# Performance work log

Hardware: AMD Instinct MI355X
Metric: run time of the kernel (lower is better)

Reference implementation:

```python
import jax, jax.numpy as jnp
import numpy as np

H = 128          # hidden_size
GX = GY = 512    # grid_size
SW = 2           # spatial_width
NX = GX + 3 * SW # memory extent x (as in SpatialExternalMemory ctor)
NY = GY + 3 * SW
B = 512          # batch (num trajectories)
T = 64           # seq len (recurrent steps)


def setup_inputs() -> dict:
    key = jax.random.key(0)
    ks = jax.random.split(key, 9)
    stdv = 1.0 / np.sqrt(H)
    feat = jax.random.normal(ks[0], (B, T, 2), jnp.float32)
    # integer grid coords stored as floats in cols 2:4 (cast to long in forward)
    coords = jax.random.randint(ks[1], (B, T, 2), 0, GX).astype(jnp.float32)
    feature_tensor = jnp.concatenate([feat, coords], axis=-1)  # [B, T, 4]
    seq_lengths = jax.random.randint(ks[2], (B,), 1, T + 1)
    uni = lambda k, shp: jax.random.uniform(k, shp, jnp.float32, -stdv, stdv)
    return {
        "feature_tensor": feature_tensor,
        "W_ih": uni(ks[3], (4 * H, 2)),
        "b_ih": uni(ks[4], (4 * H,)),
        "W_hh": uni(ks[5], (4 * H, H)),
        "b_hh": uni(ks[6], (4 * H,)),
        "W_out": uni(ks[7], (H, 2 * H)),   # Attention.linear_out: [H, 2H]
        "b_out": uni(ks[8], (H,)),
        "seq_lengths": seq_lengths,
    }


def reference(feature_tensor, W_ih, b_ih, W_hh, b_hh, W_out, b_out, seq_lengths):
    step_idx = jnp.maximum(seq_lengths.astype(jnp.int32), 1) - 1  # [B]
    offsets = jnp.arange(-SW, SW + 1)                              # [K], K=2*SW+1
    K = 2 * SW + 1
    memory0 = jnp.zeros((NX, NY, H), jnp.float32)
    hidden0 = jnp.zeros((B, H), jnp.float32)
    last0 = jnp.zeros((B, H), jnp.float32)

    def step(carry, inp):
        hidden, memory, last = carry
        xt, t = inp                                 # xt: [B,4]
        feat = xt[:, :2]
        grid = xt[:, 2:4].astype(jnp.int32) + SW    # [B,2]
        gi = feat @ W_ih.T + b_ih                   # [B,4H]
        gh = hidden @ W_hh.T + b_hh                 # [B,4H]
        i_r, i_i, i_n, i_s = jnp.split(gi, 4, axis=1)
        h_r, h_i, h_n, h_s = jnp.split(gh, 4, axis=1)
        resetgate = jax.nn.sigmoid(i_r + h_r)
        updategate = jax.nn.sigmoid(i_i + h_i)
        spatialgate = jax.nn.sigmoid(i_s + h_s)
        newgate = jnp.tanh(i_n + resetgate * h_n)
        # --- find_nearby_grids: 5x5 neighborhood gather ---
        gx = jnp.clip(grid[:, 0], 0, NX - 1)
        gy = jnp.clip(grid[:, 1], 0, NY - 1)
        xi = jnp.clip(gx[:, None] + offsets[None, :], 0, NX - 1)   # [B,K]
        yi = jnp.clip(gy[:, None] + offsets[None, :], 0, NY - 1)   # [B,K]
        xg = jnp.broadcast_to(xi[:, :, None], (B, K, K)).reshape(B, K * K)
        yg = jnp.broadcast_to(yi[:, None, :], (B, K, K)).reshape(B, K * K)
        context = memory[xg, yg]                    # [B, K*K, H]
        # --- Attention(newgate.detach(), context) ---
        q = jax.lax.stop_gradient(newgate)
        scores = jnp.einsum('bh,bkh->bk', q, context)
        scores = jnp.where(scores == 0.0, -jnp.inf, scores)
        attn = jax.nn.softmax(scores, axis=1)
        attn = jnp.where(jnp.isnan(attn), 0.0, attn)
        mix = jnp.einsum('bk,bkh->bh', attn, context)
        atten_cs = jnp.tanh(jnp.concatenate([mix, q], axis=-1) @ W_out.T + b_out)
        curr = newgate + spatialgate * atten_cs
        out = curr + updategate * (hidden - curr)
        # --- in-cell memory write (detached, training-mode path) ---
        sd = jax.lax.stop_gradient(spatialgate)
        od = jax.lax.stop_gradient(out)
        upd = sd * memory[gx, gy] + (1.0 - sd) * od
        memory = memory.at[gx, gy].set(upd)
        last = jnp.where((step_idx == t)[:, None], out, last)
        return (out, memory, last), None

    xs = (jnp.swapaxes(feature_tensor, 0, 1), jnp.arange(T))
    (_, _, last), _ = jax.lax.scan(step, (hidden0, memory0, last0), xs)
    return last
```

## Files before the change

kernel.cpp:

```cpp
#include <hip/hip_runtime.h>
#include <hip/hip_fp16.h>
#include <math.h>

#define Hc   128
#define Bc   512
#define Tc   64
#define NXc  518
#define NCELL (518*518)
#define NEV  (Bc*Tc)
#define SWc  2


__global__ void k_build(const float* __restrict__ feat, int* __restrict__ head,
                        int* __restrict__ nxt, int* __restrict__ cellxy) {
    int gid = blockIdx.x * 256 + threadIdx.x;
    if (gid >= NEV) return;
    int b = gid >> 6, t = gid & 63;
    int base = (b * Tc + t) * 4;
    int gx = (int)feat[base + 2] + SWc;
    int gy = (int)feat[base + 3] + SWc;
    gx = min(max(gx, 0), NXc - 1);
    gy = min(max(gy, 0), NXc - 1);
    int cell = gx * NXc + gy;
    int e = t * Bc + b;
    cellxy[e] = (gx << 16) | gy;
    int old = atomicExch(&head[cell], e);
    nxt[e] = old;
}

__global__ void k_resolve(const int* __restrict__ head, const int* __restrict__ nxt,
                          const int* __restrict__ cellxy, int* __restrict__ dep) {
    int gid = blockIdx.x * 256 + threadIdx.x;
    if (gid >= NEV * 25) return;
    int r = gid / 25, k = gid - r * 25;
    int t = r & 63, b = r >> 6;
    int e0 = t * Bc + b;
    int xy = cellxy[e0];
    int gx = xy >> 16, gy = xy & 0xffff;
    int cx = gx + (k / 5) - SWc, cy = gy + (k % 5) - SWc;
    cx = min(max(cx, 0), NXc - 1);
    cy = min(max(cy, 0), NXc - 1);
    int cell = cx * NXc + cy;
    int best = -1;
    for (int e = head[cell]; e >= 0; e = nxt[e])
        if ((e >> 9) < t && e > best) best = e;
    dep[r * 25 + k] = best;
}


#define LOG2E 1.4426950408889634f
__device__ __forceinline__ float fexp(float x)  { return __builtin_amdgcn_exp2f(x * LOG2E); }
__device__ __forceinline__ float fsig(float x)  { return __builtin_amdgcn_rcpf(1.f + fexp(-x)); }
__device__ __forceinline__ float ftanh(float x) { return 1.f - 2.f * __builtin_amdgcn_rcpf(1.f + fexp(2.f * x)); }

template <int CTRL>
__device__ __forceinline__ float dppadd(float x) {
    int t = __builtin_amdgcn_update_dpp(0, __float_as_int(x), CTRL, 0xF, 0xF, true);
    return x + __int_as_float(t);
}
template <int CTRL>
__device__ __forceinline__ float dppmax(float x) {
    int t = __builtin_amdgcn_update_dpp(0, __float_as_int(x), CTRL, 0xF, 0xF, true);
    return fmaxf(x, __int_as_float(t));
}
__device__ __forceinline__ float swz16(float x) {
    return __int_as_float(__builtin_amdgcn_ds_swizzle(__float_as_int(x), 0x401F));
}
__device__ __forceinline__ float redsum64(float d) {
    d = dppadd<0xB1>(d); d = dppadd<0x4E>(d);
    d = dppadd<0x141>(d); d = dppadd<0x140>(d);
    d += swz16(d);
    d += __shfl_xor(d, 32, 64);
    return d;
}

__device__ __forceinline__ void barlds() {
    asm volatile("" ::: "memory");
    __builtin_amdgcn_s_waitcnt(0xC07F);
    __builtin_amdgcn_s_barrier();
    asm volatile("" ::: "memory");
}

__device__ __forceinline__ unsigned flagload(const unsigned* p) {
    return __hip_atomic_load(p, __ATOMIC_RELAXED, __HIP_MEMORY_SCOPE_AGENT);
}


constexpr int LDS_FLOATS = 16512 + 256 + 1024 + 256 + 256 + 64 + 2048 + 512 + 16 + 128 + 256 + 128;
constexpr int LDS_BYTES  = LDS_FLOATS * 4;

__global__ void
__attribute__((amdgpu_flat_work_group_size(1024, 1024)))
__attribute__((amdgpu_waves_per_eu(4, 4)))
step_main(const float* __restrict__ feat, const float* __restrict__ Wih,
          const float* __restrict__ bih,  const float* __restrict__ Whh,
          const float* __restrict__ bhh,  const float* __restrict__ Wout,
          const float* __restrict__ bout, const int*   __restrict__ seq,
          const int*   __restrict__ dep,  float* __restrict__ vbuf,
          unsigned*    __restrict__ flags, float* __restrict__ dout) {
    extern __shared__ float lds[];
    __half2* WoutH = (__half2*)lds;
    float* hid   = lds + 16512;
    float* g     = hid   + 256;
    float* gin   = g     + 1024;
    float* ctr   = gin   + 256;
    float* scor  = ctr   + 256;
    float* pmix  = scor  + 64;
    float* catL  = pmix  + 2048;
    float* fxy   = catL  + 512;
    float* boutL = fxy   + 16;
    float* updL  = boutL + 128;
    int*   depv  = (int*)(updL + 256);

    const int tid  = threadIdx.x;
    const int blk  = blockIdx.x;
    const int lane = tid & 63;
    const int w    = tid >> 6;
    const int wj   = w >> 3;
    const int ww   = w & 7;

    const int rp = tid >> 2;
    const int q  = tid & 3;
    const int r0 = 2 * rp, r1 = 2 * rp + 1;
    float4 wr0[8], wr1[8];
    {
        const float4* w0 = (const float4*)(Whh + (size_t)r0 * Hc);
        const float4* w1 = (const float4*)(Whh + (size_t)r1 * Hc);
        #pragma unroll
        for (int i = 0; i < 8; ++i) { wr0[i] = w0[q + 4 * i]; wr1[i] = w1[q + 4 * i]; }
    }
    #pragma unroll
    for (int i = 0; i < 8; ++i) {
        asm volatile("" : "+v"(wr0[i].x), "+v"(wr0[i].y), "+v"(wr0[i].z), "+v"(wr0[i].w));
        asm volatile("" : "+v"(wr1[i].x), "+v"(wr1[i].y), "+v"(wr1[i].z), "+v"(wr1[i].w));
    }
    const int jw = q & 1;
    const int rw = r0 + (q >> 1);
    const float bihr = bih[rw], bhhr = bhh[rw];
    const float wihA = Wih[rw * 2 + 0], wihB = Wih[rw * 2 + 1];
    const int chunk = rw >> 7;

    for (int i = tid; i < 128 * 128; i += 1024) {
        int r = i >> 7, c2 = i & 127;
        WoutH[r * 129 + c2] = __floats2half2_rn(Wout[r * 256 + 2 * c2],
                                                Wout[r * 256 + 2 * c2 + 1]);
    }
    if (tid < 128) boutL[tid] = bout[tid];
    if (tid < 256) hid[tid] = 0.f;
    if (tid < 8) { int j = tid >> 2, c = tid & 3;
                   fxy[tid] = feat[((size_t)(blk * 2 + j) * Tc + 0) * 4 + c]; }
    if (tid < 50) {
        int j = (tid >= 25), k = tid - j * 25;
        depv[tid] = dep[(((size_t)(blk * 2 + j)) * Tc + 0) * 25 + k];
    }
    const int s0 = max(seq[blk * 2 + 0], 1) - 1;
    const int s1 = max(seq[blk * 2 + 1], 1) - 1;
    __syncthreads();

    const float NEG_INF = -__builtin_inff();

    for (int t = 0; t < Tc; ++t) {
        const float* fx = fxy + (t & 1) * 8;
        int* depvCur = depv + (t & 1) * 64;
        int* depvNxt = depv + ((t + 1) & 1) * 64;

        if (t > 0 && (w == 0 || w == 2)) {
            int j = w >> 1;
            float2 u = *(const float2*)&updL[j * 128 + 2 * lane];
            unsigned long long raw; __builtin_memcpy(&raw, &u, 8);
            __hip_atomic_store((unsigned long long*)(vbuf +
                ((size_t)((t - 1) * Bc + blk * 2 + j)) * Hc + 2 * lane),
                raw, __ATOMIC_RELAXED, __HIP_MEMORY_SCOPE_AGENT);
        }
        const int mye = (lane < 25) ? depvCur[wj * 25 + lane] : -1;
        unsigned fpre = 0u;
        if (mye >= 0)
            fpre = flagload(&flags[mye]);
        unsigned long long rdymask = __ballot((mye >= 0) && (fpre != 0u));
        int evk[4]; bool rdy[4]; float2 valk[4];
        #pragma unroll
        for (int kk = 0; kk < 4; ++kk) {
            int k = ww + 8 * kk;
            evk[kk] = (k < 25) ? depvCur[wj * 25 + k] : -1;
            rdy[kk] = (evk[kk] >= 0) && ((rdymask >> k) & 1ull);
            valk[kk] = make_float2(0.f, 0.f);
        }
        asm volatile("" ::: "memory");
        #pragma unroll
        for (int kk = 0; kk < 4; ++kk)
            if (rdy[kk])
                valk[kk] = *(const float2*)(vbuf + (size_t)evk[kk] * Hc + 2 * lane);

        float a00 = 0.f, a01 = 0.f, a10 = 0.f, a11 = 0.f;
        {
            const float4* h0 = (const float4*)hid;
            const float4* h1 = (const float4*)(hid + 128);
            #pragma unroll
            for (int i = 0; i < 8; ++i) {
                float4 hv0 = h0[q + 4 * i], hv1 = h1[q + 4 * i];
                float4 w0 = wr0[i], w1 = wr1[i];
                a00 = fmaf(w0.x, hv0.x, fmaf(w0.y, hv0.y, fmaf(w0.z, hv0.z, fmaf(w0.w, hv0.w, a00))));
                a01 = fmaf(w1.x, hv0.x, fmaf(w1.y, hv0.y, fmaf(w1.z, hv0.z, fmaf(w1.w, hv0.w, a01))));
                a10 = fmaf(w0.x, hv1.x, fmaf(w0.y, hv1.y, fmaf(w0.z, hv1.z, fmaf(w0.w, hv1.w, a10))));
                a11 = fmaf(w1.x, hv1.x, fmaf(w1.y, hv1.y, fmaf(w1.z, hv1.z, fmaf(w1.w, hv1.w, a11))));
            }
        }
        a00 = dppadd<0x4E>(dppadd<0xB1>(a00));
        a01 = dppadd<0x4E>(dppadd<0xB1>(a01));
        a10 = dppadd<0x4E>(dppadd<0xB1>(a10));
        a11 = dppadd<0x4E>(dppadd<0xB1>(a11));
        {
            float mine = (q & 1) ? ((q >> 1) ? a11 : a10) : ((q >> 1) ? a01 : a00);
            float gi  = fmaf(wihA, fx[jw * 4 + 0], wihB * fx[jw * 4 + 1]);
            g[jw * 512 + rw] = mine + bhhr + ((chunk == 2) ? 0.f : (gi + bihr));
            if (chunk == 2) gin[jw * 128 + (rw & 127)] = gi + bihr;
        }
        if (tid >= 512 && tid < 562 && t + 1 < Tc) {
            int idx = tid - 512;
            int j = (idx >= 25), k = idx - j * 25;
            depvNxt[idx] = dep[(((size_t)(blk * 2 + j)) * Tc + (t + 1)) * 25 + k];
        }
        if (tid >= 960 && tid < 968 && t + 1 < Tc) {
            int idx = tid - 960, j = idx >> 2, c = idx & 3;
            fxy[((t + 1) & 1) * 8 + idx] =
                feat[((size_t)(blk * 2 + j) * Tc + (t + 1)) * 4 + c];
        }
        if (t > 0 && (w == 0 || w == 2)) {
            asm volatile("s_waitcnt vmcnt(0)" ::: "memory");
            if (lane == 0)
                __hip_atomic_store(&flags[(t - 1) * Bc + blk * 2 + (w >> 1)], 1u,
                                   __ATOMIC_RELAXED, __HIP_MEMORY_SCOPE_AGENT);
        }
        {
            bool pend = (mye >= 0) && (fpre == 0u);
            while (__any(pend)) {
                if (pend && flagload(&flags[mye]) != 0u)
                    pend = false;
                if (__any(pend)) __builtin_amdgcn_s_sleep(1);
            }
            asm volatile("" ::: "memory");
            #pragma unroll
            for (int kk = 0; kk < 4; ++kk)
                if (evk[kk] >= 0 && !rdy[kk])
                    valk[kk] = *(const float2*)(vbuf + (size_t)evk[kk] * Hc + 2 * lane);
        }
        barlds();

        float q0, q1;
        {
            float2 gr2 = *(const float2*)&g[wj * 512 + 2 * lane];
            float2 gn2 = *(const float2*)&g[wj * 512 + 256 + 2 * lane];
            float2 gi2 = *(const float2*)&gin[wj * 128 + 2 * lane];
            q0 = ftanh(gi2.x + fsig(gr2.x) * gn2.x);
            q1 = ftanh(gi2.y + fsig(gr2.y) * gn2.y);
        }
        if (ww == 0) *(float2*)&catL[wj * 256 + 128 + 2 * lane] = make_float2(q0, q1);
        if (ww == 4)
            *(float2*)&ctr[wj * 128 + 2 * lane] =
                (evk[1] >= 0) ? valk[1] : make_float2(0.f, 0.f);
        #pragma unroll
        for (int kk = 0; kk < 4; ++kk) {
            int k = ww + 8 * kk;
            if (k < 25) {
                float sc;
                if (evk[kk] >= 0) {
                    float d = fmaf(valk[kk].x, q0, valk[kk].y * q1);
                    d = redsum64(d);
                    sc = (d == 0.f) ? NEG_INF : d;
                } else sc = NEG_INF;
                if (lane == 0) scor[wj * 32 + k] = sc;
            }
        }
        barlds();

        {
            int k2 = lane & 31;
            float v = (k2 < 25) ? scor[wj * 32 + k2] : NEG_INF;
            float m = v;
            m = dppmax<0xB1>(m); m = dppmax<0x4E>(m);
            m = dppmax<0x141>(m); m = dppmax<0x140>(m);
            m = fmaxf(m, swz16(m));
            float a = 0.f;
            if (m != NEG_INF) {
                float p = (v == NEG_INF) ? 0.f : fexp(v - m);
                float s = p;
                s = dppadd<0xB1>(s); s = dppadd<0x4E>(s);
                s = dppadd<0x141>(s); s = dppadd<0x140>(s);
                s += swz16(s);
                a = p / s;
            }
            float pm0 = 0.f, pm1 = 0.f;
            #pragma unroll
            for (int kk = 0; kk < 4; ++kk) {
                int k = ww + 8 * kk;
                if (k < 25 && evk[kk] >= 0) {
                    float ak = __int_as_float(
                        __builtin_amdgcn_readlane(__float_as_int(a), k));
                    pm0 = fmaf(ak, valk[kk].x, pm0);
                    pm1 = fmaf(ak, valk[kk].y, pm1);
                }
            }
            *(float2*)&pmix[(wj * 8 + ww) * 128 + 2 * lane] = make_float2(pm0, pm1);
        }
        barlds();

        if (tid < 256) {
            int j = tid >> 7, h = tid & 127;
            float mix = 0.f;
            #pragma unroll
            for (int p = 0; p < 8; ++p) mix += pmix[(j * 8 + p) * 128 + h];
            catL[j * 256 + h] = mix;
        }
        barlds();

        {
            int oo = tid & 127, rep = tid >> 7;
            const __half2* wrow = WoutH + oo * 129 + rep * 16;
            const float4* c04 = (const float4*)(catL + rep * 32);
            const float4* c14 = (const float4*)(catL + 256 + rep * 32);
            float acc0 = 0.f, acc1 = 0.f;
            #pragma unroll
            for (int i = 0; i < 8; ++i) {
                __half2 wa = wrow[2 * i], wb = wrow[2 * i + 1];
                float wx = __low2float(wa), wy = __high2float(wa);
                float wz = __low2float(wb), wwv = __high2float(wb);
                float4 c0 = c04[i], c1 = c14[i];
                acc0 = fmaf(wx, c0.x, fmaf(wy, c0.y, fmaf(wz, c0.z, fmaf(wwv, c0.w, acc0))));
                acc1 = fmaf(wx, c1.x, fmaf(wy, c1.y, fmaf(wz, c1.z, fmaf(wwv, c1.w, acc1))));
            }
            pmix[rep * 128 + oo]       = acc0;
            pmix[(8 + rep) * 128 + oo] = acc1;
        }
        barlds();

        if (tid < 256) {
            int j = tid >> 7, h = tid & 127;
            float tot = boutL[h];
            #pragma unroll
            for (int p = 0; p < 8; ++p) tot += pmix[(j * 8 + p) * 128 + h];
            float at = ftanh(tot);
            float gr = g[j * 512 + h],       gu = g[j * 512 + 128 + h];
            float gn = g[j * 512 + 256 + h], gs = g[j * 512 + 384 + h];
            float rr = fsig(gr), uu = fsig(gu), ss = fsig(gs);
            float nn = ftanh(gin[j * 128 + h] + rr * gn);
            float hv = hid[j * 128 + h];
            float curr = fmaf(ss, at, nn);
            float outv = curr + uu * (hv - curr);
            hid[j * 128 + h] = outv;
            if (t < Tc - 1)
                updL[tid] = fmaf(ss, ctr[j * 128 + h], (1.f - ss) * outv);
            int sj = (j == 0) ? s0 : s1;
            if (sj == t) dout[(size_t)(blk * 2 + j) * Hc + h] = outv;
        }
        barlds();
    }
}


extern "C" void kernel_launch(void* const* d_in, const int* in_sizes, int n_in,
                              void* d_out, int out_size, void* d_ws, size_t ws_size,
                              hipStream_t stream) {
    const float* feat = (const float*)d_in[0];
    const float* Wih  = (const float*)d_in[1];
    const float* bih  = (const float*)d_in[2];
    const float* Whh  = (const float*)d_in[3];
    const float* bhh  = (const float*)d_in[4];
    const float* Wout = (const float*)d_in[5];
    const float* bout = (const float*)d_in[6];
    const int*   seq  = (const int*)d_in[7];

    char* ws = (char*)d_ws;
    size_t off = 0;
    auto carve = [&](size_t bytes) { char* p = ws + off; off += (bytes + 511) & ~(size_t)511; return p; };
    float*    vbuf   = (float*)   carve((size_t)NEV * Hc * 4);
    int*      head   = (int*)     carve((size_t)NCELL * 4);
    int*      nxt    = (int*)     carve((size_t)NEV * 4);
    int*      cellxy = (int*)     carve((size_t)NEV * 4);
    int*      dep    = (int*)     carve((size_t)NEV * 25 * 4);
    unsigned* flags  = (unsigned*)carve((size_t)NEV * 4);

    hipMemsetAsync(head, 0xFF, (size_t)NCELL * 4, stream);
    hipMemsetAsync(flags, 0, (size_t)NEV * 4, stream);

    k_build<<<(NEV + 255) / 256, 256, 0, stream>>>(feat, head, nxt, cellxy);
    k_resolve<<<(NEV * 25 + 255) / 256, 256, 0, stream>>>(head, nxt, cellxy, dep);

    hipFuncSetAttribute((const void*)step_main,
                        hipFuncAttributeMaxDynamicSharedMemorySize, LDS_BYTES);
    step_main<<<256, 1024, LDS_BYTES, stream>>>(feat, Wih, bih, Whh, bhh, Wout, bout,
                                                seq, dep, vbuf, flags, (float*)d_out);
}
```

Measured before the change: 473.0 us.

## Keep Wout in registers, regroup Whh matvec, atomically accumulate attention mix

The fp16 copy of W_out moves from LDS into per-thread registers, and the W_hh matvec is regrouped so each thread holds four rows over eight-lane groups with a three-step DPP reduction. The attention mix partials are now summed with LDS atomicAdd into catL, which removes one reduction pass and one barrier per step. The speculative early loading of ready neighbour values before the matvec is dropped, so all vbuf loads happen after the dependency wait. The change lowers LDS traffic and footprint and trims a barrier, but raises register pressure and adds LDS atomic contention.

```diff
diff --git a/kernel.cpp b/kernel.cpp
--- a/kernel.cpp
+++ b/kernel.cpp
@@ -73,6 +73,10 @@
     d += __shfl_xor(d, 32, 64);
     return d;
 }
+__device__ __forceinline__ float redsum8(float d) {
+    d = dppadd<0xB1>(d); d = dppadd<0x4E>(d); d = dppadd<0x141>(d);
+    return d;
+}
 
 __device__ __forceinline__ void barlds() {
     asm volatile("" ::: "memory");
@@ -86,7 +90,7 @@
 }
 
 
-constexpr int LDS_FLOATS = 16512 + 256 + 1024 + 256 + 256 + 64 + 2048 + 512 + 16 + 128 + 256 + 128;
+constexpr int LDS_FLOATS = 256 + 1024 + 256 + 256 + 64 + 2048 + 512 + 16 + 256 + 128;
 constexpr int LDS_BYTES  = LDS_FLOATS * 4;
 
 __global__ void
@@ -99,8 +103,7 @@
           const int*   __restrict__ dep,  float* __restrict__ vbuf,
           unsigned*    __restrict__ flags, float* __restrict__ dout) {
     extern __shared__ float lds[];
-    __half2* WoutH = (__half2*)lds;
-    float* hid   = lds + 16512;
+    float* hid   = lds;
     float* g     = hid   + 256;
     float* gin   = g     + 1024;
     float* ctr   = gin   + 256;
@@ -108,8 +111,7 @@
     float* pmix  = scor  + 64;
     float* catL  = pmix  + 2048;
     float* fxy   = catL  + 512;
-    float* boutL = fxy   + 16;
-    float* updL  = boutL + 128;
+    float* updL  = fxy   + 16;
     int*   depv  = (int*)(updL + 256);
 
     const int tid  = threadIdx.x;
@@ -119,33 +121,44 @@
     const int wj   = w >> 3;
     const int ww   = w & 7;
 
-    const int rp = tid >> 2;
-    const int q  = tid & 3;
-    const int r0 = 2 * rp, r1 = 2 * rp + 1;
-    float4 wr0[8], wr1[8];
+    const int grp = tid >> 3;
+    const int s   = tid & 7;
+    float4 wrr[4][4];
     {
-        const float4* w0 = (const float4*)(Whh + (size_t)r0 * Hc);
-        const float4* w1 = (const float4*)(Whh + (size_t)r1 * Hc);
-        #pragma unroll
-        for (int i = 0; i < 8; ++i) { wr0[i] = w0[q + 4 * i]; wr1[i] = w1[q + 4 * i]; }
+        const float4* wb = (const float4*)Whh;
+        #pragma unroll
+        for (int r = 0; r < 4; ++r)
+            #pragma unroll
+            for (int i = 0; i < 4; ++i)
+                wrr[r][i] = wb[(size_t)(4 * grp + r) * 32 + s + 8 * i];
     }
     #pragma unroll
-    for (int i = 0; i < 8; ++i) {
-        asm volatile("" : "+v"(wr0[i].x), "+v"(wr0[i].y), "+v"(wr0[i].z), "+v"(wr0[i].w));
-        asm volatile("" : "+v"(wr1[i].x), "+v"(wr1[i].y), "+v"(wr1[i].z), "+v"(wr1[i].w));
+    for (int r = 0; r < 4; ++r)
+        #pragma unroll
+        for (int i = 0; i < 4; ++i)
+            asm volatile("" : "+v"(wrr[r][i].x), "+v"(wrr[r][i].y),
+                              "+v"(wrr[r][i].z), "+v"(wrr[r][i].w));
+
+    const int jwl = s >> 2;
+    const int rwl = 4 * grp + (s & 3);
+    const float bihr = bih[rwl], bhhr = bhh[rwl];
+    const float wihA = Wih[rwl * 2 + 0], wihB = Wih[rwl * 2 + 1];
+    const int chunk = rwl >> 7;
+
+    const int oo7 = tid & 127, rep7 = tid >> 7;
+    unsigned wo[16];
+    {
+        const float* wrow = Wout + (size_t)oo7 * 256 + rep7 * 32;
+        #pragma unroll
+        for (int m = 0; m < 16; ++m) {
+            __half2 hh = __floats2half2_rn(wrow[2 * m], wrow[2 * m + 1]);
+            unsigned u; __builtin_memcpy(&u, &hh, 4);
+            wo[m] = u;
+            asm volatile("" : "+v"(wo[m]));
+        }
     }
-    const int jw = q & 1;
-    const int rw = r0 + (q >> 1);
-    const float bihr = bih[rw], bhhr = bhh[rw];
-    const float wihA = Wih[rw * 2 + 0], wihB = Wih[rw * 2 + 1];
-    const int chunk = rw >> 7;
-
-    for (int i = tid; i < 128 * 128; i += 1024) {
-        int r = i >> 7, c2 = i & 127;
-        WoutH[r * 129 + c2] = __floats2half2_rn(Wout[r * 256 + 2 * c2],
-                                                Wout[r * 256 + 2 * c2 + 1]);
-    }
-    if (tid < 128) boutL[tid] = bout[tid];
+    const float boutr = bout[oo7];
+
     if (tid < 256) hid[tid] = 0.f;
     if (tid < 8) { int j = tid >> 2, c = tid & 3;
                    fxy[tid] = feat[((size_t)(blk * 2 + j) * Tc + 0) * 4 + c]; }
@@ -173,47 +186,41 @@
                 raw, __ATOMIC_RELAXED, __HIP_MEMORY_SCOPE_AGENT);
         }
         const int mye = (lane < 25) ? depvCur[wj * 25 + lane] : -1;
-        unsigned fpre = 0u;
+        unsigned fpre = 1u;
         if (mye >= 0)
             fpre = flagload(&flags[mye]);
-        unsigned long long rdymask = __ballot((mye >= 0) && (fpre != 0u));
-        int evk[4]; bool rdy[4]; float2 valk[4];
-        #pragma unroll
-        for (int kk = 0; kk < 4; ++kk) {
-            int k = ww + 8 * kk;
-            evk[kk] = (k < 25) ? depvCur[wj * 25 + k] : -1;
-            rdy[kk] = (evk[kk] >= 0) && ((rdymask >> k) & 1ull);
-            valk[kk] = make_float2(0.f, 0.f);
-        }
-        asm volatile("" ::: "memory");
-        #pragma unroll
-        for (int kk = 0; kk < 4; ++kk)
-            if (rdy[kk])
-                valk[kk] = *(const float2*)(vbuf + (size_t)evk[kk] * Hc + 2 * lane);
-
-        float a00 = 0.f, a01 = 0.f, a10 = 0.f, a11 = 0.f;
+
+        float acc[2][4];
+        #pragma unroll
+        for (int j = 0; j < 2; ++j) {
+            const float4* hp = (const float4*)(hid + j * 128);
+            float4 h0 = hp[s], h1 = hp[s + 8], h2 = hp[s + 16], h3 = hp[s + 24];
+            #pragma unroll
+            for (int r = 0; r < 4; ++r) {
+                float4 w0 = wrr[r][0], w1 = wrr[r][1], w2 = wrr[r][2], w3 = wrr[r][3];
+                float a = 0.f;
+                a = fmaf(w0.x, h0.x, fmaf(w0.y, h0.y, fmaf(w0.z, h0.z, fmaf(w0.w, h0.w, a))));
+                a = fmaf(w1.x, h1.x, fmaf(w1.y, h1.y, fmaf(w1.z, h1.z, fmaf(w1.w, h1.w, a))));
+                a = fmaf(w2.x, h2.x, fmaf(w2.y, h2.y, fmaf(w2.z, h2.z, fmaf(w2.w, h2.w, a))));
+                a = fmaf(w3.x, h3.x, fmaf(w3.y, h3.y, fmaf(w3.z, h3.z, fmaf(w3.w, h3.w, a))));
+                acc[j][r] = a;
+            }
+        }
+        #pragma unroll
+        for (int j = 0; j < 2; ++j)
+            #pragma unroll
+            for (int r = 0; r < 4; ++r)
+                acc[j][r] = redsum8(acc[j][r]);
         {
-            const float4* h0 = (const float4*)hid;
-            const float4* h1 = (const float4*)(hid + 128);
-            #pragma unroll
-            for (int i = 0; i < 8; ++i) {
-                float4 hv0 = h0[q + 4 * i], hv1 = h1[q + 4 * i];
-                float4 w0 = wr0[i], w1 = wr1[i];
-                a00 = fmaf(w0.x, hv0.x, fmaf(w0.y, hv0.y, fmaf(w0.z, hv0.z, fmaf(w0.w, hv0.w, a00))));
-                a01 = fmaf(w1.x, hv0.x, fmaf(w1.y, hv0.y, fmaf(w1.z, hv0.z, fmaf(w1.w, hv0.w, a01))));
-                a10 = fmaf(w0.x, hv1.x, fmaf(w0.y, hv1.y, fmaf(w0.z, hv1.z, fmaf(w0.w, hv1.w, a10))));
-                a11 = fmaf(w1.x, hv1.x, fmaf(w1.y, hv1.y, fmaf(w1.z, hv1.z, fmaf(w1.w, hv1.w, a11))));
-            }
-        }
-        a00 = dppadd<0x4E>(dppadd<0xB1>(a00));
-        a01 = dppadd<0x4E>(dppadd<0xB1>(a01));
-        a10 = dppadd<0x4E>(dppadd<0xB1>(a10));
-        a11 = dppadd<0x4E>(dppadd<0xB1>(a11));
-        {
-            float mine = (q & 1) ? ((q >> 1) ? a11 : a10) : ((q >> 1) ? a01 : a00);
-            float gi  = fmaf(wihA, fx[jw * 4 + 0], wihB * fx[jw * 4 + 1]);
-            g[jw * 512 + rw] = mine + bhhr + ((chunk == 2) ? 0.f : (gi + bihr));
-            if (chunk == 2) gin[jw * 128 + (rw & 127)] = gi + bihr;
+            int sb = s & 3;
+            float m0 = (sb == 0) ? acc[0][0] : (sb == 1) ? acc[0][1]
+                     : (sb == 2) ? acc[0][2] : acc[0][3];
+            float m1 = (sb == 0) ? acc[1][0] : (sb == 1) ? acc[1][1]
+                     : (sb == 2) ? acc[1][2] : acc[1][3];
+            float mine = jwl ? m1 : m0;
+            float gi = fmaf(wihA, fx[jwl * 4 + 0], wihB * fx[jwl * 4 + 1]);
+            g[jwl * 512 + rwl] = mine + bhhr + ((chunk == 2) ? 0.f : (gi + bihr));
+            if (chunk == 2) gin[jwl * 128 + (rwl & 127)] = gi + bihr;
         }
         if (tid >= 512 && tid < 562 && t + 1 < Tc) {
             int idx = tid - 512;
@@ -238,11 +245,17 @@
                     pend = false;
                 if (__any(pend)) __builtin_amdgcn_s_sleep(1);
             }
-            asm volatile("" ::: "memory");
-            #pragma unroll
-            for (int kk = 0; kk < 4; ++kk)
-                if (evk[kk] >= 0 && !rdy[kk])
-                    valk[kk] = *(const float2*)(vbuf + (size_t)evk[kk] * Hc + 2 * lane);
+        }
+        asm volatile("" ::: "memory");
+        float2 valk[4];
+        int    evk[4];
+        #pragma unroll
+        for (int kk = 0; kk < 4; ++kk) {
+            int k = ww + 8 * kk;
+            evk[kk] = (k < 25) ? depvCur[wj * 25 + k] : -1;
+            valk[kk] = make_float2(0.f, 0.f);
+            if (evk[kk] >= 0)
+                valk[kk] = *(const float2*)(vbuf + (size_t)evk[kk] * Hc + 2 * lane);
         }
         barlds();
 
@@ -255,6 +268,7 @@
             q1 = ftanh(gi2.y + fsig(gr2.y) * gn2.y);
         }
         if (ww == 0) *(float2*)&catL[wj * 256 + 128 + 2 * lane] = make_float2(q0, q1);
+        if (ww == 1) *(float2*)&catL[wj * 256 + 2 * lane] = make_float2(0.f, 0.f);
         if (ww == 4)
             *(float2*)&ctr[wj * 128 + 2 * lane] =
                 (evk[1] >= 0) ? valk[1] : make_float2(0.f, 0.f);
@@ -283,59 +297,53 @@
             float a = 0.f;
             if (m != NEG_INF) {
                 float p = (v == NEG_INF) ? 0.f : fexp(v - m);
-                float s = p;
-                s = dppadd<0xB1>(s); s = dppadd<0x4E>(s);
-                s = dppadd<0x141>(s); s = dppadd<0x140>(s);
-                s += swz16(s);
-                a = p / s;
-            }
-            float pm0 = 0.f, pm1 = 0.f;
-            #pragma unroll
-            for (int kk = 0; kk < 4; ++kk) {
-                int k = ww + 8 * kk;
-                if (k < 25 && evk[kk] >= 0) {
-                    float ak = __int_as_float(
-                        __builtin_amdgcn_readlane(__float_as_int(a), k));
-                    pm0 = fmaf(ak, valk[kk].x, pm0);
-                    pm1 = fmaf(ak, valk[kk].y, pm1);
+                float ssum = p;
+                ssum = dppadd<0xB1>(ssum); ssum = dppadd<0x4E>(ssum);
+                ssum = dppadd<0x141>(ssum); ssum = dppadd<0x140>(ssum);
+                ssum += swz16(ssum);
+                a = p / ssum;
+            }
+            if ((evk[0] >= 0) | (evk[1] >= 0) | (evk[2] >= 0) | (evk[3] >= 0)) {
+                float pm0 = 0.f, pm1 = 0.f;
+                #pragma unroll
+                for (int kk = 0; kk < 4; ++kk) {
+                    int k = ww + 8 * kk;
+                    if (k < 25 && evk[kk] >= 0) {
+                        float ak = __int_as_float(
+                            __builtin_amdgcn_readlane(__float_as_int(a), k));
+                        pm0 = fmaf(ak, valk[kk].x, pm0);
+                        pm1 = fmaf(ak, valk[kk].y, pm1);
+                    }
                 }
-            }
-            *(float2*)&pmix[(wj * 8 + ww) * 128 + 2 * lane] = make_float2(pm0, pm1);
+                atomicAdd(&catL[wj * 256 + 2 * lane],     pm0);
+                atomicAdd(&catL[wj * 256 + 2 * lane + 1], pm1);
+            }
         }
         barlds();
 
-        if (tid < 256) {
-            int j = tid >> 7, h = tid & 127;
-            float mix = 0.f;
-            #pragma unroll
-            for (int p = 0; p < 8; ++p) mix += pmix[(j * 8 + p) * 128 + h];
-            catL[j * 256 + h] = mix;
-        }
-        barlds();
-
         {
-            int oo = tid & 127, rep = tid >> 7;
-            const __half2* wrow = WoutH + oo * 129 + rep * 16;
-            const float4* c04 = (const float4*)(catL + rep * 32);
-            const float4* c14 = (const float4*)(catL + 256 + rep * 32);
+            const float4* c04 = (const float4*)(catL + rep7 * 32);
+            const float4* c14 = (const float4*)(catL + 256 + rep7 * 32);
             float acc0 = 0.f, acc1 = 0.f;
             #pragma unroll
             for (int i = 0; i < 8; ++i) {
-                __half2 wa = wrow[2 * i], wb = wrow[2 * i + 1];
+                unsigned ua = wo[2 * i], ub = wo[2 * i + 1];
+                __half2 wa, wb2;
+                __builtin_memcpy(&wa, &ua, 4); __builtin_memcpy(&wb2, &ub, 4);
                 float wx = __low2float(wa), wy = __high2float(wa);
-                float wz = __low2float(wb), wwv = __high2float(wb);
+                float wz = __low2float(wb2), wv = __high2float(wb2);
                 float4 c0 = c04[i], c1 = c14[i];
-                acc0 = fmaf(wx, c0.x, fmaf(wy, c0.y, fmaf(wz, c0.z, fmaf(wwv, c0.w, acc0))));
-                acc1 = fmaf(wx, c1.x, fmaf(wy, c1.y, fmaf(wz, c1.z, fmaf(wwv, c1.w, acc1))));
-            }
-            pmix[rep * 128 + oo]       = acc0;
-            pmix[(8 + rep) * 128 + oo] = acc1;
+                acc0 = fmaf(wx, c0.x, fmaf(wy, c0.y, fmaf(wz, c0.z, fmaf(wv, c0.w, acc0))));
+                acc1 = fmaf(wx, c1.x, fmaf(wy, c1.y, fmaf(wz, c1.z, fmaf(wv, c1.w, acc1))));
+            }
+            pmix[rep7 * 128 + oo7]       = acc0;
+            pmix[(8 + rep7) * 128 + oo7] = acc1;
         }
         barlds();
 
         if (tid < 256) {
             int j = tid >> 7, h = tid & 127;
-            float tot = boutL[h];
+            float tot = boutr;
             #pragma unroll
             for (int p = 0; p < 8; ++p) tot += pmix[(j * 8 + p) * 128 + h];
             float at = ftanh(tot);
```

New measurement: 486.0 us. 2.8% more time.
